# Kernel tuning notes

Measured on AMD Instinct MI355X. Metric: run time of the kernel, lower is better.

The kernel has to match this reference:

```python
import jax, jax.numpy as jnp
import numpy as np

B, S, H = 64, 4096, 512

def setup_inputs() -> dict:
    key = jax.random.key(0)
    ks = jax.random.split(key, 8)
    decoder_output = jax.random.normal(ks[0], (B, H), dtype=jnp.float32)
    encoder_output = jax.random.normal(ks[1], (B, S, 2 * H), dtype=jnp.float32)
    mask = jax.random.randint(ks[2], (B, S), 0, 2).astype(bool)
    mask = mask.at[:, 0].set(True)  # guarantee at least one valid position per row
    sc_h = 1.0 / np.sqrt(2 * H)
    sc_s = 1.0 / np.sqrt(H)
    W_h_w = jax.random.uniform(ks[3], (H, 2 * H), jnp.float32, -sc_h, sc_h)
    W_h_b = jax.random.uniform(ks[4], (H,), jnp.float32, -sc_h, sc_h)
    W_s_w = jax.random.uniform(ks[5], (H, H), jnp.float32, -sc_s, sc_s)
    W_s_b = jax.random.uniform(ks[6], (H,), jnp.float32, -sc_s, sc_s)
    v_w = jax.random.uniform(ks[7], (1, H), jnp.float32, -sc_s, sc_s)
    return {"decoder_output": decoder_output, "encoder_output": encoder_output,
            "mask": mask, "W_h_w": W_h_w, "W_h_b": W_h_b,
            "W_s_w": W_s_w, "W_s_b": W_s_b, "v_w": v_w}

def reference(decoder_output, encoder_output, mask, W_h_w, W_h_b, W_s_w, W_s_b, v_w):
    # enc proj: [B,S,H]; dec proj: [B,H] broadcast over S
    enc = jnp.einsum('bse,he->bsh', encoder_output, W_h_w) + W_h_b
    dec = decoder_output @ W_s_w.T + W_s_b  # [B,H]
    x = jnp.tanh(enc + dec[:, None, :])     # [B,S,H]
    scores = jnp.einsum('bsh,h->bs', x, v_w[0])  # [B,S]
    masked = jnp.where(mask, scores, -jnp.inf)
    return jax.nn.softmax(masked, axis=-1)
```

## Files before the change

kernel.cpp:

```cpp
#include <hip/hip_runtime.h>
#include <math.h>

typedef __attribute__((ext_vector_type(8))) short bf16x8;
typedef __attribute__((ext_vector_type(4))) float f32x4;
typedef __attribute__((ext_vector_type(4))) unsigned short u16x4;

#define NB 64
#define NS 4096
#define NH 512
#define NE 1024

__device__ __forceinline__ unsigned short f2bf(float f) {
  unsigned int u = __float_as_uint(f);
  u += 0x7fffu + ((u >> 16) & 1u);
  return (unsigned short)(u >> 16);
}

__device__ __forceinline__ float fast_tanh(float x) {
  float e = __expf(2.0f * x);
  return 1.0f - 2.0f * __builtin_amdgcn_rcpf(e + 1.0f);
}

__global__ __launch_bounds__(256) void prep_b_kernel(const float* __restrict__ W,
                                                     unsigned short* __restrict__ Bp) {
  const int t = blockIdx.x * 256 + threadIdx.x;
  const int lane = t & 63;
  const int ni = (t >> 6) & 3;
  const int kb = (t >> 8) & 31;
  const int w = t >> 13;
  const int col = w * 64 + ni * 16 + (lane & 15);
  const int k0 = kb * 32 + (lane >> 4) * 8;
  const float* src = W + col * NE + k0;
  float4 a = *(const float4*)src;
  float4 b = *(const float4*)(src + 4);
  union { bf16x8 v; unsigned short u[8]; } p;
  p.u[0] = f2bf(a.x); p.u[1] = f2bf(a.y); p.u[2] = f2bf(a.z); p.u[3] = f2bf(a.w);
  p.u[4] = f2bf(b.x); p.u[5] = f2bf(b.y); p.u[6] = f2bf(b.z); p.u[7] = f2bf(b.w);
  *(bf16x8*)(Bp + (long long)t * 8) = p.v;
}

__global__ __launch_bounds__(512) void prep_dec_kernel(const float* __restrict__ dec,
                                                       const float* __restrict__ Wsw,
                                                       const float* __restrict__ Wsb,
                                                       const float* __restrict__ Whb,
                                                       float* __restrict__ decb) {
  int b = blockIdx.x;
  int h = threadIdx.x;
  const float4* dr = (const float4*)(dec + b * NH);
  const float4* wr = (const float4*)(Wsw + h * NH);
  float sum = Wsb[h] + Whb[h];
#pragma unroll 8
  for (int i = 0; i < NH / 4; ++i) {
    float4 a = dr[i], w = wr[i];
    sum += a.x * w.x + a.y * w.y + a.z * w.z + a.w * w.w;
  }
  decb[b * NH + h] = sum;
}

__global__ __launch_bounds__(512, 4) void fused_main(const float* __restrict__ enc,
                                                     const unsigned short* __restrict__ Bp,
                                                     const float* __restrict__ decb,
                                                     const float* __restrict__ vw,
                                                     float* __restrict__ scores) {
  __shared__ __align__(16) float As[3][2048];
  __shared__ float ssc[64];

  const int tid = threadIdx.x;
  const int lane = tid & 63;
  const int wave = tid >> 6;
  const int r15 = lane & 15;
  const int c4 = lane >> 4;
  const long long m0 = (long long)blockIdx.x * 64;

  if (tid < 64) ssc[tid] = 0.0f;

  const int grow = wave * 8 + (lane >> 3);
  const int ggran = (lane & 7) ^ (lane >> 3);
  const float* gsrc = enc + (m0 + grow) * NE + ggran * 4;
  const unsigned ldsoff = wave * 1024;

  const int rowb = r15 * 128;
  const int pg0 = (((c4 << 1) | 0) ^ (lane & 7)) << 4;
  const int pg1 = (((c4 << 1) | 1) ^ (lane & 7)) << 4;

  const unsigned short* const bb = Bp + (long long)wave * 32 * 2048 + lane * 8;

  f32x4 acc[4][4];
#pragma unroll
  for (int mi = 0; mi < 4; ++mi)
#pragma unroll
    for (int ni = 0; ni < 4; ++ni) {
      f32x4 z = {0.f, 0.f, 0.f, 0.f};
      acc[mi][ni] = z;
    }

  bf16x8 bcur[4];
#pragma unroll
  for (int ni = 0; ni < 4; ++ni) bcur[ni] = *(const bf16x8*)(bb + ni * 512);
  __builtin_amdgcn_global_load_lds((const unsigned int*)gsrc,
                                   (unsigned int*)((char*)&As[0][0] + ldsoff), 16, 0, 0);
  __builtin_amdgcn_global_load_lds((const unsigned int*)(gsrc + 32),
                                   (unsigned int*)((char*)&As[1][0] + ldsoff), 16, 0, 0);
  asm volatile("s_waitcnt vmcnt(1)" ::: "memory");
  __builtin_amdgcn_s_barrier();

#pragma unroll
  for (int t = 0; t < 32; ++t) {
    const char* Ab = (const char*)&As[t % 3][0];
    bf16x8 af[4];
#pragma unroll
    for (int mi = 0; mi < 4; ++mi) {
      f32x4 lo = *(const f32x4*)(Ab + mi * 2048 + rowb + pg0);
      f32x4 hi = *(const f32x4*)(Ab + mi * 2048 + rowb + pg1);
      union { unsigned int u[4]; bf16x8 v; } pk;
      asm("v_cvt_pk_bf16_f32 %0, %1, %2" : "=v"(pk.u[0]) : "v"(lo.x), "v"(lo.y));
      asm("v_cvt_pk_bf16_f32 %0, %1, %2" : "=v"(pk.u[1]) : "v"(lo.z), "v"(lo.w));
      asm("v_cvt_pk_bf16_f32 %0, %1, %2" : "=v"(pk.u[2]) : "v"(hi.x), "v"(hi.y));
      asm("v_cvt_pk_bf16_f32 %0, %1, %2" : "=v"(pk.u[3]) : "v"(hi.z), "v"(hi.w));
      af[mi] = pk.v;
    }
    __builtin_amdgcn_s_setprio(1);
#pragma unroll
    for (int mi = 0; mi < 4; ++mi)
#pragma unroll
      for (int ni = 0; ni < 4; ++ni)
        acc[mi][ni] = __builtin_amdgcn_mfma_f32_16x16x32_bf16(af[mi], bcur[ni],
                                                              acc[mi][ni], 0, 0, 0);
    __builtin_amdgcn_s_setprio(0);
    if (t < 31) {
      const unsigned short* bp = bb + (t + 1) * 2048;
#pragma unroll
      for (int ni = 0; ni < 4; ++ni) bcur[ni] = *(const bf16x8*)(bp + ni * 512);
    }
    if (t < 30)
      __builtin_amdgcn_global_load_lds((const unsigned int*)(gsrc + (t + 2) * 32),
                                       (unsigned int*)((char*)&As[(t + 2) % 3][0] + ldsoff),
                                       16, 0, 0);
    if (t < 31) {
      if (t < 30) asm volatile("s_waitcnt vmcnt(5)" ::: "memory");
      else        asm volatile("s_waitcnt vmcnt(4)" ::: "memory");
      asm volatile("s_waitcnt lgkmcnt(0)" ::: "memory");
      __builtin_amdgcn_sched_barrier(0);
      __builtin_amdgcn_s_barrier();
    }
  }

  const int bidx = (int)(m0 >> 12);
  const float* decrow = decb + bidx * NH;
  float part[4][4];
#pragma unroll
  for (int mi = 0; mi < 4; ++mi)
#pragma unroll
    for (int j = 0; j < 4; ++j) part[mi][j] = 0.f;

#pragma unroll
  for (int ni = 0; ni < 4; ++ni) {
    int col = (wave << 6) + ni * 16 + r15;
    float vc = vw[col];
    float dc = decrow[col];
#pragma unroll
    for (int mi = 0; mi < 4; ++mi)
#pragma unroll
      for (int j = 0; j < 4; ++j)
        part[mi][j] += vc * fast_tanh(acc[mi][ni][j] + dc);
  }
#pragma unroll
  for (int off = 1; off < 16; off <<= 1)
#pragma unroll
    for (int mi = 0; mi < 4; ++mi)
#pragma unroll
      for (int j = 0; j < 4; ++j)
        part[mi][j] += __shfl_xor(part[mi][j], off, 64);

  if (r15 == 0) {
#pragma unroll
    for (int mi = 0; mi < 4; ++mi)
#pragma unroll
      for (int j = 0; j < 4; ++j)
        atomicAdd(&ssc[mi * 16 + c4 * 4 + j], part[mi][j]);
  }
  __syncthreads();
  if (tid < 64) scores[m0 + tid] = ssc[tid];
}

__global__ __launch_bounds__(1024) void softmax_kernel(const float* __restrict__ scores,
                                                       const int* __restrict__ mask,
                                                       float* __restrict__ out) {
  __shared__ float rmax[16];
  __shared__ float rsum[16];
  const int b = blockIdx.x;
  const int t = threadIdx.x;
  const int wid = t >> 6;
  const int ln = t & 63;
  const int base = b * NS;

  float s[4];
  int mk[4];
  float mx = -INFINITY;
#pragma unroll
  for (int i = 0; i < 4; ++i) {
    int idx = t + i * 1024;
    s[i] = scores[base + idx];
    mk[i] = mask[base + idx];
    if (mk[i]) mx = fmaxf(mx, s[i]);
  }
#pragma unroll
  for (int off = 1; off < 64; off <<= 1) mx = fmaxf(mx, __shfl_xor(mx, off, 64));
  if (ln == 0) rmax[wid] = mx;
  __syncthreads();
  float m2 = -INFINITY;
#pragma unroll
  for (int i = 0; i < 16; ++i) m2 = fmaxf(m2, rmax[i]);

  float e[4];
  float sum = 0.f;
#pragma unroll
  for (int i = 0; i < 4; ++i) {
    e[i] = mk[i] ? expf(s[i] - m2) : 0.f;
    sum += e[i];
  }
#pragma unroll
  for (int off = 1; off < 64; off <<= 1) sum += __shfl_xor(sum, off, 64);
  if (ln == 0) rsum[wid] = sum;
  __syncthreads();
  float tot = 0.f;
#pragma unroll
  for (int i = 0; i < 16; ++i) tot += rsum[i];
  float inv = 1.0f / tot;
#pragma unroll
  for (int i = 0; i < 4; ++i) {
    int idx = t + i * 1024;
    out[base + idx] = e[i] * inv;
  }
}

extern "C" void kernel_launch(void* const* d_in, const int* in_sizes, int n_in,
                              void* d_out, int out_size, void* d_ws, size_t ws_size,
                              hipStream_t stream) {
  const float* dec = (const float*)d_in[0];
  const float* enc = (const float*)d_in[1];
  const int* mask = (const int*)d_in[2];
  const float* Whw = (const float*)d_in[3];
  const float* Whb = (const float*)d_in[4];
  const float* Wsw = (const float*)d_in[5];
  const float* Wsb = (const float*)d_in[6];
  const float* vw = (const float*)d_in[7];
  float* out = (float*)d_out;

  unsigned short* Bp = (unsigned short*)d_ws;
  float* decb = (float*)((char*)d_ws + (1 << 20));
  float* scoresb = (float*)((char*)d_ws + (1 << 20) + (128 << 10));

  prep_b_kernel<<<dim3(256), dim3(256), 0, stream>>>(Whw, Bp);
  prep_dec_kernel<<<dim3(64), dim3(512), 0, stream>>>(dec, Wsw, Wsb, Whb, decb);
  fused_main<<<dim3(4096), dim3(512), 0, stream>>>(enc, Bp, decb, vw, scoresb);
  softmax_kernel<<<dim3(64), dim3(1024), 0, stream>>>(scoresb, mask, out);
}
```

Before: 449.0 us.

## Deepen A prefetch to four LDS stages and interleave per-row MFMA phases

Grows the LDS ring for the fp32 encoder tiles from three to four stages, so three tiles are in flight, and double-buffers the bf16 weight fragments in registers, alternating between two sets. Each k-step is split into four phases, one per 16-row sub-tile. Each phase reads and converts one A fragment and then issues its four MFMAs, with barriers placed between phases. The goal is to hide global and LDS latency behind matrix work. In exchange it adds more barriers per iteration, extra LDS and extra register pressure, which could hurt occupancy at four blocks per CU.

```diff
diff --git a/kernel.cpp b/kernel.cpp
--- a/kernel.cpp
+++ b/kernel.cpp
@@ -62,7 +62,7 @@
                                                      const float* __restrict__ decb,
                                                      const float* __restrict__ vw,
                                                      float* __restrict__ scores) {
-  __shared__ __align__(16) float As[3][2048];
+  __shared__ __align__(16) float As[4][2048];
   __shared__ float ssc[64];
 
   const int tid = threadIdx.x;
@@ -94,54 +94,77 @@
       acc[mi][ni] = z;
     }
 
-  bf16x8 bcur[4];
-#pragma unroll
-  for (int ni = 0; ni < 4; ++ni) bcur[ni] = *(const bf16x8*)(bb + ni * 512);
   __builtin_amdgcn_global_load_lds((const unsigned int*)gsrc,
                                    (unsigned int*)((char*)&As[0][0] + ldsoff), 16, 0, 0);
   __builtin_amdgcn_global_load_lds((const unsigned int*)(gsrc + 32),
                                    (unsigned int*)((char*)&As[1][0] + ldsoff), 16, 0, 0);
-  asm volatile("s_waitcnt vmcnt(1)" ::: "memory");
-  __builtin_amdgcn_s_barrier();
+  __builtin_amdgcn_global_load_lds((const unsigned int*)(gsrc + 64),
+                                   (unsigned int*)((char*)&As[2][0] + ldsoff), 16, 0, 0);
+  bf16x8 bA[4], bB[4];
+#pragma unroll
+  for (int ni = 0; ni < 4; ++ni) bA[ni] = *(const bf16x8*)(bb + ni * 512);
 
 #pragma unroll
   for (int t = 0; t < 32; ++t) {
-    const char* Ab = (const char*)&As[t % 3][0];
-    bf16x8 af[4];
-#pragma unroll
-    for (int mi = 0; mi < 4; ++mi) {
-      f32x4 lo = *(const f32x4*)(Ab + mi * 2048 + rowb + pg0);
-      f32x4 hi = *(const f32x4*)(Ab + mi * 2048 + rowb + pg1);
-      union { unsigned int u[4]; bf16x8 v; } pk;
-      asm("v_cvt_pk_bf16_f32 %0, %1, %2" : "=v"(pk.u[0]) : "v"(lo.x), "v"(lo.y));
-      asm("v_cvt_pk_bf16_f32 %0, %1, %2" : "=v"(pk.u[1]) : "v"(lo.z), "v"(lo.w));
-      asm("v_cvt_pk_bf16_f32 %0, %1, %2" : "=v"(pk.u[2]) : "v"(hi.x), "v"(hi.y));
-      asm("v_cvt_pk_bf16_f32 %0, %1, %2" : "=v"(pk.u[3]) : "v"(hi.z), "v"(hi.w));
-      af[mi] = pk.v;
-    }
-    __builtin_amdgcn_s_setprio(1);
-#pragma unroll
-    for (int mi = 0; mi < 4; ++mi)
-#pragma unroll
-      for (int ni = 0; ni < 4; ++ni)
-        acc[mi][ni] = __builtin_amdgcn_mfma_f32_16x16x32_bf16(af[mi], bcur[ni],
-                                                              acc[mi][ni], 0, 0, 0);
-    __builtin_amdgcn_s_setprio(0);
-    if (t < 31) {
-      const unsigned short* bp = bb + (t + 1) * 2048;
-#pragma unroll
-      for (int ni = 0; ni < 4; ++ni) bcur[ni] = *(const bf16x8*)(bp + ni * 512);
-    }
-    if (t < 30)
-      __builtin_amdgcn_global_load_lds((const unsigned int*)(gsrc + (t + 2) * 32),
-                                       (unsigned int*)((char*)&As[(t + 2) % 3][0] + ldsoff),
-                                       16, 0, 0);
-    if (t < 31) {
-      if (t < 30) asm volatile("s_waitcnt vmcnt(5)" ::: "memory");
-      else        asm volatile("s_waitcnt vmcnt(4)" ::: "memory");
-      asm volatile("s_waitcnt lgkmcnt(0)" ::: "memory");
-      __builtin_amdgcn_sched_barrier(0);
-      __builtin_amdgcn_s_barrier();
+    const char* Ab = (const char*)&As[t & 3][0];
+#pragma unroll
+    for (int p = 0; p < 4; ++p) {
+      bf16x8 af;
+      if (p == 0) {
+        if (t < 31) {
+          const bf16x8* bp = (const bf16x8*)(bb + (t + 1) * 2048);
+          if (t & 1) {
+#pragma unroll
+            for (int ni = 0; ni < 4; ++ni) bA[ni] = bp[ni * 64];
+          } else {
+#pragma unroll
+            for (int ni = 0; ni < 4; ++ni) bB[ni] = bp[ni * 64];
+          }
+        }
+        if (t < 29)
+          __builtin_amdgcn_global_load_lds((const unsigned int*)(gsrc + (t + 3) * 32),
+                                           (unsigned int*)((char*)&As[(t + 3) & 3][0] + ldsoff),
+                                           16, 0, 0);
+        if (t == 0)       asm volatile("s_waitcnt vmcnt(5)" ::: "memory");
+        else if (t < 29)  asm volatile("s_waitcnt vmcnt(6)" ::: "memory");
+        else if (t == 29) asm volatile("s_waitcnt vmcnt(5)" ::: "memory");
+        else if (t == 30) asm volatile("s_waitcnt vmcnt(4)" ::: "memory");
+        else              asm volatile("s_waitcnt vmcnt(0)" ::: "memory");
+        __builtin_amdgcn_s_barrier();
+        f32x4 lo = *(const f32x4*)(Ab + rowb + pg0);
+        f32x4 hi = *(const f32x4*)(Ab + rowb + pg1);
+        asm volatile("s_waitcnt lgkmcnt(0)" ::: "memory");
+        __builtin_amdgcn_sched_barrier(0);
+        union { unsigned int u[4]; bf16x8 v; } pk;
+        asm("v_cvt_pk_bf16_f32 %0, %1, %2" : "=v"(pk.u[0]) : "v"(lo.x), "v"(lo.y));
+        asm("v_cvt_pk_bf16_f32 %0, %1, %2" : "=v"(pk.u[1]) : "v"(lo.z), "v"(lo.w));
+        asm("v_cvt_pk_bf16_f32 %0, %1, %2" : "=v"(pk.u[2]) : "v"(hi.x), "v"(hi.y));
+        asm("v_cvt_pk_bf16_f32 %0, %1, %2" : "=v"(pk.u[3]) : "v"(hi.z), "v"(hi.w));
+        af = pk.v;
+      } else {
+        f32x4 lo = *(const f32x4*)(Ab + p * 2048 + rowb + pg0);
+        f32x4 hi = *(const f32x4*)(Ab + p * 2048 + rowb + pg1);
+        asm volatile("s_waitcnt lgkmcnt(0)" ::: "memory");
+        __builtin_amdgcn_sched_barrier(0);
+        union { unsigned int u[4]; bf16x8 v; } pk;
+        asm("v_cvt_pk_bf16_f32 %0, %1, %2" : "=v"(pk.u[0]) : "v"(lo.x), "v"(lo.y));
+        asm("v_cvt_pk_bf16_f32 %0, %1, %2" : "=v"(pk.u[1]) : "v"(lo.z), "v"(lo.w));
+        asm("v_cvt_pk_bf16_f32 %0, %1, %2" : "=v"(pk.u[2]) : "v"(hi.x), "v"(hi.y));
+        asm("v_cvt_pk_bf16_f32 %0, %1, %2" : "=v"(pk.u[3]) : "v"(hi.z), "v"(hi.w));
+        af = pk.v;
+        __builtin_amdgcn_s_barrier();
+      }
+      __builtin_amdgcn_s_setprio(1);
+      if (t & 1) {
+#pragma unroll
+        for (int ni = 0; ni < 4; ++ni)
+          acc[p][ni] = __builtin_amdgcn_mfma_f32_16x16x32_bf16(af, bB[ni], acc[p][ni], 0, 0, 0);
+      } else {
+#pragma unroll
+        for (int ni = 0; ni < 4; ++ni)
+          acc[p][ni] = __builtin_amdgcn_mfma_f32_16x16x32_bf16(af, bA[ni], acc[p][ni], 0, 0, 0);
+      }
+      __builtin_amdgcn_s_setprio(0);
     }
   }
 
```

Measured after the change: 459.3 us. 1.02x slower.
